# Kernel optimization log

Hardware: AMD Instinct MI355X
Metric: run time of the kernel (lower is better)

The kernel has to match this reference:

```python
import jax, jax.numpy as jnp
import numpy as np
from jax.scipy.special import xlogy

LAMBDA_XM = 0.05
LAMBDA_SEG2D = 1.0
BN_EPS = 1e-5


def setup_inputs() -> dict:
    key = jax.random.key(0)
    ks = jax.random.split(key, 40)
    S, N, Nv, B, Np, M, H, C, MID = 2, 240000, 80000, 2, 120000, 30000, 64, 20, 16
    Nimg = B * M
    f = lambda i, shape, s=0.05: jax.random.normal(ks[i], shape, jnp.float32) * s
    inp = {
        'img_feat': f(0, (S, Nimg, H), 1.0),
        'pts_feat': f(1, (S, Nv, H), 1.0),
        'coors_inv': jax.random.randint(ks[2], (S, N), 0, Nv),
        'labels': jax.random.randint(ks[3], (N,), 0, C),
        'img_label': jax.random.randint(ks[4], (Nimg,), 0, C),
        'p2img_idx': jax.random.randint(ks[5], (B, M), 0, Np),
        # multihead 3d classifiers (per scale): Linear(H,128)-ReLU-Linear(128,C)
        'w3a': f(6, (S, H, 128)), 'b3a': jnp.zeros((S, 128)),
        'w3b': f(7, (S, 128, C)), 'b3b': jnp.zeros((S, C)),
        # multihead fuse classifiers
        'wfa': f(8, (S, H, 128)), 'bfa': jnp.zeros((S, 128)),
        'wfb': f(9, (S, 128, C)), 'bfb': jnp.zeros((S, C)),
        # attention: fc1(H->H//4), fc2(H->H//4), fc3(H//2->2), conv1/conv2 (1x1 -> linear) + BN
        'fc1w': f(10, (S, H, MID)), 'fc1b': jnp.zeros((S, MID)),
        'fc2w': f(11, (S, H, MID)), 'fc2b': jnp.zeros((S, MID)),
        'fc3w': f(12, (S, 2 * MID, 2)), 'fc3b': jnp.zeros((S, 2)),
        'c1w': f(13, (S, H, H)), 'c1b': jnp.zeros((S, H)),
        'bn1g': jnp.ones((S, H)), 'bn1b': jnp.zeros((S, H)),
        'c2w': f(14, (S, H, H)), 'c2b': jnp.zeros((S, H)),
        'bn2g': jnp.ones((S, H)), 'bn2b': jnp.zeros((S, H)),
        # final classifier Linear(S*H,128)-ReLU-Linear(128,C)
        'clw1': f(15, (S * H, 128)), 'clb1': jnp.zeros((128,)),
        'clw2': f(16, (128, C)), 'clb2': jnp.zeros((C,)),
    }
    return inp


def _mlp2(x, w1, b1, w2, b2):
    return jax.nn.relu(x @ w1 + b1) @ w2 + b2


def _ce(logits, lab):
    logp = jax.nn.log_softmax(logits, -1)
    return -jnp.take_along_axis(logp, lab[:, None], axis=1).mean()


def _lovasz(probs, lab):
    # lovasz-softmax over all classes, averaged over present classes
    C = probs.shape[1]
    fg = jax.nn.one_hot(lab, C, dtype=probs.dtype)  # [N,C]
    errors = jnp.abs(fg - probs)

    def per_class(err_c, fg_c):
        order = jnp.argsort(-err_c)
        e = err_c[order]
        f = fg_c[order]
        gts = f.sum()
        inter = gts - jnp.cumsum(f)
        union = gts + jnp.cumsum(1.0 - f)
        jac = 1.0 - inter / union
        jac = jnp.concatenate([jac[:1], jac[1:] - jac[:-1]])
        return jnp.dot(e, jac)

    losses = jax.vmap(per_class)(errors.T, fg.T)  # [C]
    present = (fg.sum(0) > 0).astype(probs.dtype)
    return jnp.sum(losses * present) / jnp.maximum(present.sum(), 1.0)


def _seg_loss(logits, lab):
    return _ce(logits, lab) + _lovasz(jax.nn.softmax(logits, -1), lab)


def _convbn_relu(x, cw, cb, g, b):
    # 1x1 Conv1d == per-point linear; BN (training-mode batch stats over points)
    y = x @ cw + cb
    mu = y.mean(0)
    var = y.var(0)
    return jax.nn.relu((y - mu) * jax.lax.rsqrt(var + BN_EPS) * g + b)


def reference(img_feat, pts_feat, coors_inv, labels, img_label, p2img_idx,
              w3a, b3a, w3b, b3b, wfa, bfa, wfb, bfb,
              fc1w, fc1b, fc2w, fc2b, fc3w, fc3b,
              c1w, c1b, bn1g, bn1b, c2w, c2b, bn2g, bn2b,
              clw1, clb1, clw2, clb2):
    S, Nv, H = pts_feat.shape
    C = w3b.shape[-1]
    B, M = p2img_idx.shape
    N = labels.shape[0]
    Np = N // B
    # p2img_mapping: per-batch gather composed to one global gather (batch blocks are contiguous/equal)
    gidx = (jnp.arange(B)[:, None] * Np + p2img_idx).reshape(-1)  # [Nimg]

    loss = jnp.float32(0.0)
    feats = []
    for s in range(S):
        pred3d = _mlp2(pts_feat[s], w3a[s], b3a[s], w3b[s], b3b[s])  # [Nv,C]
        # voxelize_labels: majority vote per voxel (== unique+scatter_max count argmax)
        counts = jnp.zeros((Nv, C), jnp.float32).at[coors_inv[s], labels].add(1.0)
        vox_lab = jnp.argmax(counts, axis=1)  # [Nv]
        # gather voxel feats/preds to image-projected points (fused gather)
        idx = coors_inv[s][gidx]  # [Nimg]
        p = pts_feat[s][idx]      # [Nimg,H] pseudo feats
        pts_pred = pred3d[idx]    # [Nimg,C]
        v = img_feat[s]           # [Nimg,H] valid (image) feats
        # Attention fusion
        w = jax.nn.sigmoid(
            jnp.concatenate([p @ fc1w[s] + fc1b[s], v @ fc2w[s] + fc2b[s]], -1) @ fc3w[s] + fc3b[s])  # [Nimg,2]
        fuse = (_convbn_relu(p, c1w[s], c1b[s], bn1g[s], bn1b[s]) * w[:, 0:1]
                + _convbn_relu(v, c2w[s], c2b[s], bn2g[s], bn2b[s]) * w[:, 1:2])
        feats.append(fuse)
        fuse_pred = _mlp2(fuse, wfa[s], bfa[s], wfb[s], bfb[s])
        loss = loss + _seg_loss(pred3d, vox_lab)
        loss = loss + _seg_loss(fuse_pred, img_label) * LAMBDA_SEG2D / S
        # F.kl_div(log_softmax(pts_pred), softmax(fuse_pred)), reduction='mean' over all elements
        pf = jax.nn.softmax(fuse_pred, -1)
        kl = jnp.mean(xlogy(pf, pf) - pf * jax.nn.log_softmax(pts_pred, -1))
        loss = loss + kl * LAMBDA_XM / S
    img_logits = _mlp2(jnp.concatenate(feats, -1), clw1, clb1, clw2, clb2)
    loss = loss + _seg_loss(img_logits, img_label)
    return loss
```

## Files before the change

kernel.cpp:

```cpp
#include <hip/hip_runtime.h>
#include <stdint.h>

static constexpr int NV   = 80000;
static constexpr int NPT  = 240000;
static constexpr int NIMG = 60000;
static constexpr int Hh   = 64;
static constexpr int Cc   = 20;
static constexpr int NPp  = 120000;
static constexpr int Mm   = 30000;
static constexpr int NB     = 8192;
static constexpr int NCH    = 16;
static constexpr int NBLK_GA  = (NIMG + 63) / 64;
static constexpr int NBLK_MLP = NV / 64;
static constexpr int NBLK_CNT = (NPT + 255) / 256;
static constexpr int NBLK_FILL_NV = (NV + 255) / 256;
static constexpr int NBLK_FILL_NI = (NIMG + 255) / 256;
static constexpr int NBLK_HIST = Cc * NCH;
static constexpr int NBLK_GATH = 2 * NIMG * 8 / 256;
static constexpr int NBLK_P3G  = (2 * NIMG + 255) / 256;
#define BN_EPS 1e-5f

using bf16x8 = __attribute__((ext_vector_type(8))) short;
using f32x4  = __attribute__((ext_vector_type(4))) float;

__device__ __forceinline__ float waveReduce(float v) {
  #pragma unroll
  for (int o = 32; o > 0; o >>= 1) v += __shfl_down(v, o);
  return v;
}
__device__ __forceinline__ short f2bf(float f) {
  uint32_t u = __float_as_uint(f);
  return (short)((u + 0x7FFFu + ((u >> 16) & 1u)) >> 16);
}
__device__ __forceinline__ float bf2f(uint32_t h) { return __uint_as_float(h << 16); }
__device__ __forceinline__ uint32_t pk2(float a, float b) {
  return ((uint32_t)(uint16_t)f2bf(a)) | ((uint32_t)(uint16_t)f2bf(b) << 16);
}

struct PackDesc { const float* src; short* dst; int K, Nr, nt; };
struct PackArgs { PackDesc d[14]; };

__global__ void __launch_bounds__(256)
k_pack_zero(PackArgs pa,
            const float* __restrict__ fc1w, const float* __restrict__ fc1b,
            const float* __restrict__ fc2w, const float* __restrict__ fc2b,
            const float* __restrict__ fc3w, const float* __restrict__ fc3b,
            float* __restrict__ attEffs,
            uint4* __restrict__ zb, int zq,
            const int* __restrict__ ci0, const int* __restrict__ ci1,
            const int* __restrict__ p2img,
            int* __restrict__ idx0, int* __restrict__ idx1,
            const float* __restrict__ pts, uint16_t* __restrict__ pgath) {
  int bid = blockIdx.x;
  if (bid >= 384) {
    int g = (bid - 384) * 256 + threadIdx.x;
    int row = g >> 3, q = g & 7;
    int r = (row >= NIMG) ? row - NIMG : row;
    int s1 = (row >= NIMG) ? 1 : 0;
    const int* ci = s1 ? ci1 : ci0;
    int b = (r >= Mm) ? 1 : 0;
    int id = ci[b * NPp + p2img[r]];
    if (q == 0) { if (s1) idx1[r] = id; else idx0[r] = id; }
    const float* src = pts + (size_t)s1 * NV * 64 + (size_t)id * 64 + q * 8;
    float4 a = *(const float4*)src;
    float4 c = *(const float4*)(src + 4);
    uint4 o;
    o.x = pk2(a.x, a.y); o.y = pk2(a.z, a.w);
    o.z = pk2(c.x, c.y); o.w = pk2(c.z, c.w);
    *(uint4*)(pgath + (size_t)row * 64 + q * 8) = o;
    return;
  }
  if (bid >= 128) {
    const uint4 z = make_uint4(0u, 0u, 0u, 0u);
    int i = (bid - 128) * 256 + threadIdx.x;
    for (; i < zq; i += 256 * 256) zb[i] = z;
    return;
  }
  const int stride = 128 * 256;
  for (int di = 0; di < 14; di++) {
    const float* src = pa.d[di].src;
    short* dst = pa.d[di].dst;
    int K = pa.d[di].K, Nr = pa.d[di].Nr, ntiles = pa.d[di].nt;
    int total = (K / 32) * ntiles * 512;
    for (int idx = bid * 256 + threadIdx.x; idx < total; idx += stride) {
      int j = idx & 7, lane = (idx >> 3) & 63, tile = idx >> 9;
      int nt = tile % ntiles, kt = tile / ntiles;
      int k = kt * 32 + (lane >> 4) * 8 + j;
      int n = nt * 16 + (lane & 15);
      float v = (n < Nr) ? src[(size_t)k * Nr + n] : 0.f;
      dst[idx] = f2bf(v);
    }
  }
  if (bid < 2 && threadIdx.x < 64) {
    int s = bid, t = threadIdx.x;
    const float* f1w = fc1w + s * 64 * 16; const float* f1b = fc1b + s * 16;
    const float* f2w = fc2w + s * 64 * 16; const float* f2b = fc2b + s * 16;
    const float* f3w = fc3w + s * 64;      const float* f3b = fc3b + s * 2;
    float* aE = attEffs + s * 320;
    float p0 = 0.f, p1 = 0.f, v0 = 0.f, v1 = 0.f;
    #pragma unroll
    for (int j = 0; j < 16; j++) {
      p0 = fmaf(f1w[t * 16 + j], f3w[j * 2], p0);
      p1 = fmaf(f1w[t * 16 + j], f3w[j * 2 + 1], p1);
      v0 = fmaf(f2w[t * 16 + j], f3w[(16 + j) * 2], v0);
      v1 = fmaf(f2w[t * 16 + j], f3w[(16 + j) * 2 + 1], v1);
    }
    aE[t * 2] = p0; aE[t * 2 + 1] = p1;
    aE[128 + t * 2] = v0; aE[128 + t * 2 + 1] = v1;
    if (t == 0) {
      float b0 = f3b[0], b1 = f3b[1];
      for (int j = 0; j < 16; j++) {
        b0 += f1b[j] * f3w[j * 2] + f2b[j] * f3w[(16 + j) * 2];
        b1 += f1b[j] * f3w[j * 2 + 1] + f2b[j] * f3w[(16 + j) * 2 + 1];
      }
      aE[256] = b0; aE[257] = b1;
    }
  }
}

__device__ void scanbin_body(const unsigned long long* __restrict__ H64,
                             int n, int call, float* __restrict__ lossesC5,
                             int* __restrict__ gts5, int cls) {
  __shared__ int sWC[4], sWF[4];
  __shared__ float sRedF[4];
  int t = threadIdx.x;
  int lane = t & 63, w = t >> 6;
  const uint4* Hv = (const uint4*)(H64 + (size_t)cls * NB + (size_t)t * 32);
  int locC = 0, locF = 0;
  #pragma unroll
  for (int i = 0; i < 16; i++) {
    uint4 u = Hv[i];
    locF += (int)(u.x + u.z);
    locC += (int)(u.y + u.w);
  }
  int sc = locC, sf = locF;
  #pragma unroll
  for (int o = 1; o < 64; o <<= 1) {
    int a = __shfl_up(sc, o);
    int b = __shfl_up(sf, o);
    if (lane >= o) { sc += a; sf += b; }
  }
  if (lane == 63) { sWC[w] = sc; sWF[w] = sf; }
  __syncthreads();
  int offC = 0, offF = 0, Ftot = 0;
  #pragma unroll
  for (int ww = 0; ww < 4; ww++) {
    int fc = sWF[ww];
    Ftot += fc;
    if (ww < w) { offC += sWC[ww]; offF += fc; }
  }
  int runC = offC + sc - locC;
  int runF = offF + sf - locF;
  float gts = (float)Ftot;
  float contrib = 0.f;
  #pragma unroll
  for (int i = 0; i < 16; i++) {
    uint4 u = Hv[i];
    #pragma unroll
    for (int j = 0; j < 2; j++) {
      int cnt = (int)(j ? u.w : u.y), fgc = (int)(j ? u.z : u.x);
      runC += cnt; runF += fgc;
      if (cnt > 0 && Ftot > 0) {
        float r0 = (float)(n - runC);
        float F0 = (float)(Ftot - runF);
        float r1 = r0 + (float)cnt;
        float F1 = F0 + (float)fgc;
        float emean = __uint_as_float((uint32_t)(t * 32 + i * 2 + j) << 17);
        contrib += emean * (r1 / (gts + r1 - F1) - r0 / (gts + r0 - F0));
      }
    }
  }
  contrib = waveReduce(contrib);
  if (lane == 0) sRedF[w] = contrib;
  __syncthreads();
  if (t == 0) {
    lossesC5[call * 32 + cls] = (Ftot > 0) ? (sRedF[0] + sRedF[1] + sRedF[2] + sRedF[3]) : 0.f;
    gts5[call * 32 + cls] = Ftot;
  }
}

__device__ void tile_loss(const float* __restrict__ sL, int r0, int rows, int n,
                          const int* __restrict__ lab, uint16_t* __restrict__ E,
                          float ceScale, float* __restrict__ lossAcc) {
  int t = threadIdx.x;
  if (t < 64) {
    float total = 0.f;
    int gr = r0 + t;
    if (gr < rows) {
      const float* l = sL + t * 21;
      float m = l[0];
      #pragma unroll
      for (int c = 1; c < Cc; c++) m = fmaxf(m, l[c]);
      float ex[Cc]; float se = 0.f;
      #pragma unroll
      for (int c = 0; c < Cc; c++) { ex[c] = expf(l[c] - m); se += ex[c]; }
      float inv = 1.f / se;
      float lse = logf(se);
      int lb = lab[gr];
      total = -(l[lb] - m - lse) * ceScale;
      #pragma unroll
      for (int c = 0; c < Cc; c++) {
        float prob = ex[c] * inv;
        int fg = (c == lb) ? 1 : 0;
        float err = fg ? (1.f - prob) : prob;
        err = fmaxf(err, 0.f);
        uint32_t key = __float_as_uint(err) >> 17;
        E[(size_t)c * n + gr] = (uint16_t)((key << 1) | (uint32_t)fg);
      }
    }
    total = waveReduce(total);
    if (t == 0) atomicAdd(lossAcc, total);
  }
}

template<int D, bool TO_LDS>
__device__ __forceinline__ void mfma_mlp_core(const short* sXb, short* sH, float* sL,
    int r0, int rows,
    const short* __restrict__ pw1, const float* __restrict__ B1,
    const short* __restrict__ pw2, const float* __restrict__ B2,
    float* __restrict__ Out) {
  constexpr int LDB = D + 8;
  constexpr int KT1 = D / 32;
  const int t = threadIdx.x;
  const int lane = t & 63, w = t >> 6;
  const int m = lane & 15, quad = lane >> 4;
  const int rowA = 16 * w + m;
  bf16x8 a1[KT1];
  #pragma unroll
  for (int kt = 0; kt < KT1; kt++)
    a1[kt] = *(const bf16x8*)(sXb + rowA * LDB + kt * 32 + quad * 8);
  __syncthreads();
  const bf16x8* b1 = (const bf16x8*)pw1;
  #pragma unroll
  for (int nt = 0; nt < 8; nt++) {
    f32x4 c = {0.f, 0.f, 0.f, 0.f};
    #pragma unroll
    for (int kt = 0; kt < KT1; kt++)
      c = __builtin_amdgcn_mfma_f32_16x16x32_bf16(a1[kt], b1[(kt * 8 + nt) * 64 + lane], c, 0, 0, 0);
    int col = nt * 16 + m;
    float bc = B1[col];
    #pragma unroll
    for (int reg = 0; reg < 4; reg++)
      sH[(16 * w + quad * 4 + reg) * 136 + col] = f2bf(fmaxf(c[reg] + bc, 0.f));
  }
  __syncthreads();
  bf16x8 a2[4];
  #pragma unroll
  for (int kt = 0; kt < 4; kt++)
    a2[kt] = *(const bf16x8*)(sH + rowA * 136 + kt * 32 + quad * 8);
  if (TO_LDS) __syncthreads();
  const bf16x8* b2 = (const bf16x8*)pw2;
  #pragma unroll
  for (int nt = 0; nt < 2; nt++) {
    f32x4 c = {0.f, 0.f, 0.f, 0.f};
    #pragma unroll
    for (int kt = 0; kt < 4; kt++)
      c = __builtin_amdgcn_mfma_f32_16x16x32_bf16(a2[kt], b2[(kt * 2 + nt) * 64 + lane], c, 0, 0, 0);
    int col = nt * 16 + m;
    if (col < Cc) {
      float bc = B2[col];
      #pragma unroll
      for (int reg = 0; reg < 4; reg++) {
        int rr = 16 * w + quad * 4 + reg;
        if (TO_LDS) {
          sL[rr * 21 + col] = c[reg] + bc;
        } else {
          int gr = r0 + rr;
          if (gr < rows) Out[(size_t)gr * Cc + col] = c[reg] + bc;
        }
      }
    }
  }
}

__device__ void mlp64_body(int bid0, const float* __restrict__ X,
    const short* __restrict__ pw1, const float* __restrict__ B1,
    const short* __restrict__ pw2, const float* __restrict__ B2,
    float* __restrict__ Out, int rows, char* smem) {
  short* buf = (short*)smem;
  int t = threadIdx.x, r0 = bid0 * 64;
  for (int i = t; i < 1024; i += 256) {
    int r = i >> 4, k4 = (i & 15) * 4;
    int gr = r0 + r;
    float4 v = (gr < rows) ? *(const float4*)(X + (size_t)gr * 64 + k4)
                           : make_float4(0.f, 0.f, 0.f, 0.f);
    uint2 p; p.x = pk2(v.x, v.y); p.y = pk2(v.z, v.w);
    *(uint2*)(buf + r * 72 + k4) = p;
  }
  __syncthreads();
  mfma_mlp_core<64, false>(buf, buf, nullptr, r0, rows, pw1, B1, pw2, B2, Out);
}

__device__ void mlp128_loss_body(int bid0, const uint16_t* __restrict__ Xh,
    const short* __restrict__ pw1, const float* __restrict__ B1,
    const short* __restrict__ pw2, const float* __restrict__ B2,
    const int* __restrict__ lab, uint16_t* __restrict__ E, float ce,
    float* __restrict__ lossAcc, char* smem) {
  short* buf = (short*)smem;
  int t = threadIdx.x, r0 = bid0 * 64;
  for (int i = t; i < 2048; i += 256) {
    int r = i >> 5, k4 = (i & 31) * 4;
    int gr = r0 + r;
    uint2 p = (gr < NIMG) ? *(const uint2*)(Xh + (size_t)gr * 128 + k4) : make_uint2(0u, 0u);
    *(uint2*)(buf + r * 136 + k4) = p;
  }
  __syncthreads();
  mfma_mlp_core<128, true>(buf, buf, (float*)buf, r0, NIMG, pw1, B1, pw2, B2, nullptr);
  __syncthreads();
  tile_loss((float*)buf, r0, NIMG, NIMG, lab, E, ce, lossAcc);
}

__device__ void cnt_body(int bid0, const int* __restrict__ ci, const int* __restrict__ labels,
                         int* __restrict__ counts) {
  int i = bid0 * 256 + threadIdx.x;
  if (i < NPT) atomicAdd(&counts[(size_t)ci[i] * Cc + labels[i]], 1);
}

__device__ void colred_body(int bid0, const float* __restrict__ partials,
                            float* __restrict__ red64) {
  int t = threadIdx.x, j = bid0;
  float v = 0.f;
  for (int b = j; b < NBLK_GA; b += 64) v += partials[(size_t)b * 256 + t];
  red64[j * 256 + t] = v;
}

__device__ void p3gath_body(int bid0, const float* __restrict__ pred3d0,
                            const float* __restrict__ pred3d1,
                            const int* __restrict__ idx0, const int* __restrict__ idx1,
                            float* __restrict__ p3g0, float* __restrict__ p3g1) {
  int row = bid0 * 256 + threadIdx.x;
  if (row >= 2 * NIMG) return;
  int s1 = (row >= NIMG) ? 1 : 0;
  int r = s1 ? row - NIMG : row;
  const float* pred = s1 ? pred3d1 : pred3d0;
  float* dst = (s1 ? p3g1 : p3g0) + (size_t)r * Cc;
  const float* src = pred + (size_t)(s1 ? idx1[r] : idx0[r]) * Cc;
  #pragma unroll
  for (int c = 0; c < Cc; c += 2) {
    uint2 v = *(const uint2*)(src + c);
    *(uint2*)(dst + c) = v;
  }
}

__device__ void fill_body(int bid0, const float* __restrict__ logits,
                          const int* __restrict__ lab, const int* __restrict__ vcnt,
                          int n, uint16_t* __restrict__ E,
                          float ceScale, float* __restrict__ lossAcc,
                          const float* __restrict__ p3g, float klScale) {
  int i = bid0 * 256 + threadIdx.x;
  float total = 0.f;
  if (i < n) {
    int lb;
    if (vcnt) {
      const int* crow = vcnt + (size_t)i * Cc;
      int best = crow[0], arg = 0;
      #pragma unroll
      for (int k = 1; k < Cc; k++) {
        int ck = crow[k];
        if (ck > best) { best = ck; arg = k; }
      }
      lb = arg;
    } else {
      lb = lab[i];
    }
    const float* l = logits + (size_t)i * Cc;
    float m = l[0];
    #pragma unroll
    for (int c = 1; c < Cc; c++) m = fmaxf(m, l[c]);
    float ex[Cc]; float se = 0.f;
    #pragma unroll
    for (int c = 0; c < Cc; c++) { ex[c] = expf(l[c] - m); se += ex[c]; }
    float inv = 1.f / se;
    float lse = logf(se);
    total = -(l[lb] - m - lse) * ceScale;
    #pragma unroll
    for (int c = 0; c < Cc; c++) {
      float prob = ex[c] * inv;
      int fg = (c == lb) ? 1 : 0;
      float err = fg ? (1.f - prob) : prob;
      err = fmaxf(err, 0.f);
      uint32_t key = __float_as_uint(err) >> 17;
      E[(size_t)c * n + i] = (uint16_t)((key << 1) | (uint32_t)fg);
    }
    if (p3g) {
      const float* q = p3g + (size_t)i * Cc;
      float mq = q[0];
      #pragma unroll
      for (int c = 1; c < Cc; c++) mq = fmaxf(mq, q[c]);
      float sq = 0.f;
      #pragma unroll
      for (int c = 0; c < Cc; c++) sq += expf(q[c] - mq);
      float lsq = logf(sq);
      float kl = 0.f;
      #pragma unroll
      for (int c = 0; c < Cc; c++) {
        float lf = l[c] - m - lse;
        float pf = ex[c] * inv;
        float lq = q[c] - mq - lsq;
        kl += pf * (lf - lq);
      }
      total += kl * klScale;
    }
  }
  total = waveReduce(total);
  __shared__ float sh[4];
  int lane = threadIdx.x & 63, w = threadIdx.x >> 6;
  if (lane == 0) sh[w] = total;
  __syncthreads();
  if (threadIdx.x == 0) atomicAdd(lossAcc, sh[0] + sh[1] + sh[2] + sh[3]);
}

__device__ void hist_body(int bid0, const uint16_t* __restrict__ E, int n,
                          unsigned long long* __restrict__ H64, char* smem) {
  uint32_t* lcf = (uint32_t*)smem;
  int t = threadIdx.x;
  int cls = bid0 / NCH, ch = bid0 - cls * NCH;
  int CHsz = (n + NCH - 1) / NCH;
  int i0 = ch * CHsz;
  int i1 = min(n, i0 + CHsz);
  for (int b = t; b < NB; b += 256) lcf[b] = 0u;
  __syncthreads();
  const uint16_t* Ec = E + (size_t)cls * n;
  for (int i = i0 + t; i < i1; i += 256) {
    uint32_t p = Ec[i];
    atomicAdd(&lcf[p >> 1], 0x10000u | (p & 1u));
  }
  __syncthreads();
  unsigned long long* Hc = H64 + (size_t)cls * NB;
  for (int b = t; b < NB; b += 256) {
    uint32_t v = lcf[b];
    if (v)
      atomicAdd(&Hc[b], ((unsigned long long)(v >> 16) << 32) | (v & 0xFFFFu));
  }
}

__device__ void gatt_body(int bid0, const uint16_t* __restrict__ pg,
                          const float* __restrict__ img,
                          const short* __restrict__ pc1, const float* __restrict__ c1b,
                          const short* __restrict__ pc2, const float* __restrict__ c2b,
                          const float* __restrict__ attEff,
                          uint16_t* __restrict__ y1, uint16_t* __restrict__ y2,
                          float* __restrict__ attw, float* __restrict__ partials,
                          char* smem) {
  short* sP = (short*)smem;
  short* sV = (short*)(smem + 9216);
  float* sAtt  = (float*)(smem + 18432);
  float* sStat = (float*)smem;
  int t = threadIdx.x;
  int r0 = bid0 * 64;
  for (int i = t; i < 512; i += 256) {
    int r = i >> 3, q = i & 7;
    int gr = r0 + r;
    uint4 pv = make_uint4(0u, 0u, 0u, 0u);
    if (gr < NIMG) pv = *(const uint4*)(pg + (size_t)gr * 64 + q * 8);
    *(uint4*)(sP + r * 72 + q * 8) = pv;
  }
  for (int i = t; i < 1024; i += 256) {
    int r = i >> 4, q = i & 15;
    int gr = r0 + r;
    float4 vv = make_float4(0.f, 0.f, 0.f, 0.f);
    if (gr < NIMG) vv = *(const float4*)(img + (size_t)gr * 64 + q * 4);
    uint2 qv;
    qv.x = pk2(vv.x, vv.y); qv.y = pk2(vv.z, vv.w);
    *(uint2*)(sV + r * 72 + q * 4) = qv;
  }
  __syncthreads();
  {
    int r = t & 63, qq = t >> 6;
    const float* aP = attEff;
    const float* aV = attEff + 128;
    float l0 = 0.f, l1 = 0.f;
    for (int k = qq * 16; k < qq * 16 + 16; k += 4) {
      uint2 up = *(const uint2*)(sP + r * 72 + k);
      uint2 uv = *(const uint2*)(sV + r * 72 + k);
      float p0 = bf2f(up.x & 0xffff), p1 = bf2f(up.x >> 16);
      float p2 = bf2f(up.y & 0xffff), p3 = bf2f(up.y >> 16);
      float v0 = bf2f(uv.x & 0xffff), v1 = bf2f(uv.x >> 16);
      float v2 = bf2f(uv.y & 0xffff), v3 = bf2f(uv.y >> 16);
      float4 wa = *(const float4*)(aP + 2 * k);
      float4 wb = *(const float4*)(aP + 2 * k + 4);
      l0 += p0 * wa.x + p1 * wa.z + p2 * wb.x + p3 * wb.z;
      l1 += p0 * wa.y + p1 * wa.w + p2 * wb.y + p3 * wb.w;
      float4 ua = *(const float4*)(aV + 2 * k);
      float4 ub = *(const float4*)(aV + 2 * k + 4);
      l0 += v0 * ua.x + v1 * ua.z + v2 * ub.x + v3 * ub.z;
      l1 += v0 * ua.y + v1 * ua.w + v2 * ub.y + v3 * ub.w;
    }
    sAtt[r * 8 + qq * 2] = l0;
    sAtt[r * 8 + qq * 2 + 1] = l1;
  }
  const int lane = t & 63, w = t >> 6;
  const int m = lane & 15, quad = lane >> 4;
  const int rowA = 16 * w + m;
  bf16x8 ap[2], av[2];
  #pragma unroll
  for (int kt = 0; kt < 2; kt++) {
    ap[kt] = *(const bf16x8*)(sP + rowA * 72 + kt * 32 + quad * 8);
    av[kt] = *(const bf16x8*)(sV + rowA * 72 + kt * 32 + quad * 8);
  }
  __syncthreads();
  const bf16x8* b1 = (const bf16x8*)pc1;
  const bf16x8* b2 = (const bf16x8*)pc2;
  #pragma unroll
  for (int nt = 0; nt < 4; nt++) {
    int col = nt * 16 + m;
    f32x4 c1 = {0.f, 0.f, 0.f, 0.f}, c2 = {0.f, 0.f, 0.f, 0.f};
    #pragma unroll
    for (int kt = 0; kt < 2; kt++) {
      c1 = __builtin_amdgcn_mfma_f32_16x16x32_bf16(ap[kt], b1[(kt * 4 + nt) * 64 + lane], c1, 0, 0, 0);
      c2 = __builtin_amdgcn_mfma_f32_16x16x32_bf16(av[kt], b2[(kt * 4 + nt) * 64 + lane], c2, 0, 0, 0);
    }
    float bb1 = c1b[col], bb2 = c2b[col];
    float s1 = 0.f, q1 = 0.f, s2 = 0.f, q2 = 0.f;
    #pragma unroll
    for (int reg = 0; reg < 4; reg++) {
      int gr = r0 + 16 * w + quad * 4 + reg;
      if (gr < NIMG) {
        float v1 = c1[reg] + bb1, v2 = c2[reg] + bb2;
        y1[(size_t)gr * 64 + col] = (uint16_t)f2bf(v1);
        y2[(size_t)gr * 64 + col] = (uint16_t)f2bf(v2);
        s1 += v1; q1 = fmaf(v1, v1, q1);
        s2 += v2; q2 = fmaf(v2, v2, q2);
      }
    }
    s1 += __shfl_down(s1, 32); s1 += __shfl_down(s1, 16);
    q1 += __shfl_down(q1, 32); q1 += __shfl_down(q1, 16);
    s2 += __shfl_down(s2, 32); s2 += __shfl_down(s2, 16);
    q2 += __shfl_down(q2, 32); q2 += __shfl_down(q2, 16);
    if (lane < 16) {
      float* base = sStat + (w * 4 + nt) * 64 + lane;
      base[0]  = s1;
      base[16] = q1;
      base[32] = s2;
      base[48] = q2;
    }
  }
  __syncthreads();
  {
    int kind = t >> 6, col = t & 63;
    int nt = col >> 4, mm = col & 15;
    float v = 0.f;
    #pragma unroll
    for (int ww = 0; ww < 4; ww++)
      v += sStat[(ww * 4 + nt) * 64 + kind * 16 + mm];
    partials[(size_t)bid0 * 256 + kind * 64 + col] = v;
  }
  if (t < 64) {
    int gr = r0 + t;
    if (gr < NIMG) {
      float l0 = attEff[256] + sAtt[t * 8] + sAtt[t * 8 + 2] + sAtt[t * 8 + 4] + sAtt[t * 8 + 6];
      float l1 = attEff[257] + sAtt[t * 8 + 1] + sAtt[t * 8 + 3] + sAtt[t * 8 + 5] + sAtt[t * 8 + 7];
      attw[gr * 2]     = 1.f / (1.f + expf(-l0));
      attw[gr * 2 + 1] = 1.f / (1.f + expf(-l1));
    }
  }
}

__device__ void fusemlp_body(int bid0,
    const uint16_t* __restrict__ y1, const uint16_t* __restrict__ y2,
    const float* __restrict__ attw, const float* __restrict__ red64,
    const float* __restrict__ g1, const float* __restrict__ be1,
    const float* __restrict__ g2, const float* __restrict__ be2,
    uint16_t* __restrict__ feats, int s64,
    const short* __restrict__ pw1, const float* __restrict__ B1,
    const short* __restrict__ pw2, const float* __restrict__ B2,
    float* __restrict__ Out, char* smem) {
  short* buf = (short*)smem;
  float* sBn = (float*)(smem + 17408);
  int t = threadIdx.x, r0 = bid0 * 64;
  float acc = 0.f;
  #pragma unroll 8
  for (int b = 0; b < 64; b++) acc += red64[b * 256 + t];
  float* sSum = (float*)buf;
  sSum[t] = acc;
  __syncthreads();
  if (t < 64) {
    float nn = (float)NIMG;
    float mu1 = sSum[t] / nn;
    float var1 = sSum[64 + t] / nn - mu1 * mu1;
    float a1 = g1[t] / sqrtf(var1 + BN_EPS);
    sBn[t] = a1; sBn[64 + t] = be1[t] - mu1 * a1;
    float mu2 = sSum[128 + t] / nn;
    float var2 = sSum[192 + t] / nn - mu2 * mu2;
    float a2 = g2[t] / sqrtf(var2 + BN_EPS);
    sBn[128 + t] = a2; sBn[192 + t] = be2[t] - mu2 * a2;
  }
  __syncthreads();
  for (int i = t; i < 1024; i += 256) {
    int r = i >> 4, q = i & 15;
    int gr = r0 + r;
    uint2 zp = make_uint2(0u, 0u);
    if (gr < NIMG) {
      float4 a1 = *(const float4*)(sBn + q * 4);
      float4 c1 = *(const float4*)(sBn + 64 + q * 4);
      float4 a2 = *(const float4*)(sBn + 128 + q * 4);
      float4 c2 = *(const float4*)(sBn + 192 + q * 4);
      uint2 u1 = *(const uint2*)(y1 + (size_t)gr * 64 + q * 4);
      uint2 u2 = *(const uint2*)(y2 + (size_t)gr * 64 + q * 4);
      float w0 = attw[gr * 2], w1 = attw[gr * 2 + 1];
      float zx = fmaxf(fmaf(bf2f(u1.x & 0xffff), a1.x, c1.x), 0.f) * w0
               + fmaxf(fmaf(bf2f(u2.x & 0xffff), a2.x, c2.x), 0.f) * w1;
      float zy = fmaxf(fmaf(bf2f(u1.x >> 16),   a1.y, c1.y), 0.f) * w0
               + fmaxf(fmaf(bf2f(u2.x >> 16),   a2.y, c2.y), 0.f) * w1;
      float zz = fmaxf(fmaf(bf2f(u1.y & 0xffff), a1.z, c1.z), 0.f) * w0
               + fmaxf(fmaf(bf2f(u2.y & 0xffff), a2.z, c2.z), 0.f) * w1;
      float zw = fmaxf(fmaf(bf2f(u1.y >> 16),   a1.w, c1.w), 0.f) * w0
               + fmaxf(fmaf(bf2f(u2.y >> 16),   a2.w, c2.w), 0.f) * w1;
      zp.x = pk2(zx, zy); zp.y = pk2(zz, zw);
      *(uint2*)(feats + (size_t)gr * 128 + s64 + q * 4) = zp;
    }
    *(uint2*)(buf + r * 72 + q * 4) = zp;
  }
  __syncthreads();
  mfma_mlp_core<64, false>(buf, buf, nullptr, r0, NIMG, pw1, B1, pw2, B2, Out);
}

__global__ void __launch_bounds__(256)
k_mega2(const float* __restrict__ pf0, const float* __restrict__ pf1,
        const uint16_t* __restrict__ pg0, const uint16_t* __restrict__ pg1,
        const float* __restrict__ if0, const float* __restrict__ if1,
        const short* pc1w0, const short* pc1w1, const short* pc2w0, const short* pc2w1,
        const float* c1b, const float* c2b, const float* attEffs,
        uint16_t* y1a, uint16_t* y2a, uint16_t* y1b, uint16_t* y2b,
        float* attw0, float* attw1, float* partials0, float* partials1,
        const short* pw3a0, const float* b3a, const short* pw3b0, const float* b3b,
        const short* pw3a1, const short* pw3b1,
        float* pred3d0, float* pred3d1,
        const int* __restrict__ ci0, const int* __restrict__ ci1,
        const int* __restrict__ labels,
        int* __restrict__ counts0, int* __restrict__ counts1) {
  __shared__ char smem[20480];
  int bid = blockIdx.x;
  if (bid < NBLK_GA) {
    gatt_body(bid, pg0, if0, pc1w0, c1b, pc2w0, c2b, attEffs,
              y1a, y2a, attw0, partials0, smem);
    return;
  }
  bid -= NBLK_GA;
  if (bid < NBLK_GA) {
    gatt_body(bid, pg1, if1, pc1w1, c1b + 64, pc2w1, c2b + 64, attEffs + 320,
              y1b, y2b, attw1, partials1, smem);
    return;
  }
  bid -= NBLK_GA;
  if (bid < NBLK_MLP) { mlp64_body(bid, pf0, pw3a0, b3a, pw3b0, b3b, pred3d0, NV, smem); return; }
  bid -= NBLK_MLP;
  if (bid < NBLK_MLP) { mlp64_body(bid, pf1, pw3a1, b3a + 128, pw3b1, b3b + Cc, pred3d1, NV, smem); return; }
  bid -= NBLK_MLP;
  if (bid < NBLK_CNT) { cnt_body(bid, ci0, labels, counts0); return; }
  cnt_body(bid - NBLK_CNT, ci1, labels, counts1);
}

__global__ void __launch_bounds__(256)
k_colred_p3g(const float* partials0, float* red64_0,
             const float* partials1, float* red64_1,
             const float* __restrict__ pred3d0, const float* __restrict__ pred3d1,
             const int* __restrict__ idx0, const int* __restrict__ idx1,
             float* __restrict__ p3g0, float* __restrict__ p3g1) {
  int bid = blockIdx.x;
  if (bid < 64) { colred_body(bid, partials0, red64_0); return; }
  bid -= 64;
  if (bid < 64) { colred_body(bid, partials1, red64_1); return; }
  p3gath_body(bid - 64, pred3d0, pred3d1, idx0, idx1, p3g0, p3g1);
}

__global__ void __launch_bounds__(256)
k_fuse2_fill2(const uint16_t* y1a, const uint16_t* y2a, const float* attw0, const float* red64_0,
              const uint16_t* y1b, const uint16_t* y2b, const float* attw1, const float* red64_1,
              const float* bn1g, const float* bn1b, const float* bn2g, const float* bn2b,
              uint16_t* feats,
              const short* pwfa0, const float* bfa, const short* pwfb0, const float* bfb,
              const short* pwfa1, const short* pwfb1,
              float* fusepred0, float* fusepred1,
              const float* __restrict__ pred3d0, const int* __restrict__ counts0,
              uint16_t* __restrict__ E0,
              const float* __restrict__ pred3d1, const int* __restrict__ counts1,
              uint16_t* __restrict__ E1,
              float ceNV, float* lossAcc) {
  __shared__ char smem[18432];
  int bid = blockIdx.x;
  if (bid < NBLK_GA) {
    fusemlp_body(bid, y1a, y2a, attw0, red64_0, bn1g, bn1b, bn2g, bn2b, feats, 0,
                 pwfa0, bfa, pwfb0, bfb, fusepred0, smem);
    return;
  }
  bid -= NBLK_GA;
  if (bid < NBLK_GA) {
    fusemlp_body(bid, y1b, y2b, attw1, red64_1, bn1g + 64, bn1b + 64, bn2g + 64, bn2b + 64,
                 feats, 64, pwfa1, bfa + 128, pwfb1, bfb + Cc, fusepred1, smem);
    return;
  }
  bid -= NBLK_GA;
  if (bid < NBLK_FILL_NV) {
    fill_body(bid, pred3d0, nullptr, counts0, NV, E0, ceNV, lossAcc, nullptr, 0.f);
    return;
  }
  fill_body(bid - NBLK_FILL_NV, pred3d1, nullptr, counts1, NV, E1, ceNV, lossAcc, nullptr, 0.f);
}

__global__ void __launch_bounds__(256)
k_finx2(const uint16_t* __restrict__ feats,
        const short* pcl1, const float* clb1, const short* pcl2, const float* clb2,
        const int* __restrict__ img_label, uint16_t* E2, float ce4, float* lossAcc,
        const float* fusepred0, const float* p3g0, uint16_t* E3,
        const float* fusepred1, const float* p3g1, uint16_t* E4,
        float ce, float kl,
        const uint16_t* __restrict__ E0, unsigned long long* H0,
        const uint16_t* __restrict__ E1, unsigned long long* H2) {
  __shared__ char smem[32768];
  int bid = blockIdx.x;
  if (bid < NBLK_GA) {
    mlp128_loss_body(bid, feats, pcl1, clb1, pcl2, clb2, img_label, E2, ce4, lossAcc, smem);
    return;
  }
  bid -= NBLK_GA;
  if (bid < NBLK_FILL_NI) {
    fill_body(bid, fusepred0, img_label, nullptr, NIMG, E3, ce, lossAcc, p3g0, kl);
    return;
  }
  bid -= NBLK_FILL_NI;
  if (bid < NBLK_FILL_NI) {
    fill_body(bid, fusepred1, img_label, nullptr, NIMG, E4, ce, lossAcc, p3g1, kl);
    return;
  }
  bid -= NBLK_FILL_NI;
  if (bid < NBLK_HIST) { hist_body(bid, E0, NV, H0, smem); return; }
  hist_body(bid - NBLK_HIST, E1, NV, H2, smem);
}

__global__ void __launch_bounds__(256)
k_hist3_scan2(const uint16_t* __restrict__ E3, unsigned long long* H1,
              const uint16_t* __restrict__ E4, unsigned long long* H3,
              const uint16_t* __restrict__ E2, unsigned long long* H4,
              const unsigned long long* H0, const unsigned long long* H2s,
              float* lossesC5, int* gts5) {
  __shared__ char smem[32768];
  int bid = blockIdx.x;
  if (bid < NBLK_HIST) { hist_body(bid, E3, NIMG, H1, smem); return; }
  bid -= NBLK_HIST;
  if (bid < NBLK_HIST) { hist_body(bid, E4, NIMG, H3, smem); return; }
  bid -= NBLK_HIST;
  if (bid < NBLK_HIST) { hist_body(bid, E2, NIMG, H4, smem); return; }
  bid -= NBLK_HIST;
  if (bid < Cc) { scanbin_body(H0, NV, 0, lossesC5, gts5, bid); return; }
  scanbin_body(H2s, NV, 2, lossesC5, gts5, bid - Cc);
}

__global__ void __launch_bounds__(256)
k_scan3(const unsigned long long* H1, const unsigned long long* H3,
        const unsigned long long* H4,
        float* lossesC5, int* gts5) {
  int bid = blockIdx.x;
  if (bid < Cc) { scanbin_body(H1, NIMG, 1, lossesC5, gts5, bid); return; }
  bid -= Cc;
  if (bid < Cc) { scanbin_body(H3, NIMG, 3, lossesC5, gts5, bid); return; }
  scanbin_body(H4, NIMG, 4, lossesC5, gts5, bid - Cc);
}

__global__ void k_final(const float* __restrict__ lossAcc,
                        const float* __restrict__ lossesC5, const int* __restrict__ gts5,
                        float* __restrict__ out) {
  const float coefs[5] = {1.0f, 0.5f, 1.0f, 0.5f, 1.0f};
  float loss = lossAcc[0];
  for (int call = 0; call < 5; call++) {
    float s = 0.f; int np = 0;
    for (int c = 0; c < Cc; c++)
      if (gts5[call * 32 + c] > 0) { s += lossesC5[call * 32 + c]; np++; }
    loss += coefs[call] * s / (float)(np > 0 ? np : 1);
  }
  out[0] = loss;
}

extern "C" void kernel_launch(void* const* d_in, const int* in_sizes, int n_in,
                              void* d_out, int out_size, void* d_ws, size_t ws_size,
                              hipStream_t stream) {
  const float* img_feat = (const float*)d_in[0];
  const float* pts_feat = (const float*)d_in[1];
  const int* coors_inv  = (const int*)d_in[2];
  const int* labels     = (const int*)d_in[3];
  const int* img_label  = (const int*)d_in[4];
  const int* p2img      = (const int*)d_in[5];
  const float* w3a = (const float*)d_in[6];
  const float* b3a = (const float*)d_in[7];
  const float* w3b = (const float*)d_in[8];
  const float* b3b = (const float*)d_in[9];
  const float* wfa = (const float*)d_in[10];
  const float* bfa = (const float*)d_in[11];
  const float* wfb = (const float*)d_in[12];
  const float* bfb = (const float*)d_in[13];
  const float* fc1w = (const float*)d_in[14];
  const float* fc1b = (const float*)d_in[15];
  const float* fc2w = (const float*)d_in[16];
  const float* fc2b = (const float*)d_in[17];
  const float* fc3w = (const float*)d_in[18];
  const float* fc3b = (const float*)d_in[19];
  const float* c1w  = (const float*)d_in[20];
  const float* c1b  = (const float*)d_in[21];
  const float* bn1g = (const float*)d_in[22];
  const float* bn1b = (const float*)d_in[23];
  const float* c2w  = (const float*)d_in[24];
  const float* c2b  = (const float*)d_in[25];
  const float* bn2g = (const float*)d_in[26];
  const float* bn2b = (const float*)d_in[27];
  const float* clw1 = (const float*)d_in[28];
  const float* clb1 = (const float*)d_in[29];
  const float* clw2 = (const float*)d_in[30];
  const float* clb2 = (const float*)d_in[31];
  (void)in_sizes; (void)n_in; (void)out_size; (void)ws_size;

  char* ws = (char*)d_ws;
  size_t off = 0;
  auto alloc = [&](size_t bytes) { void* p = ws + off; off += (bytes + 255) & ~(size_t)255; return p; };
  uint16_t* feats = (uint16_t*)alloc((size_t)NIMG * 128 * 2);
  uint16_t* pgath = (uint16_t*)alloc((size_t)2 * NIMG * 64 * 2);
  float* pred3d0 = (float*)alloc((size_t)NV * Cc * 4);
  float* pred3d1 = (float*)alloc((size_t)NV * Cc * 4);
  float* p3g0 = (float*)alloc((size_t)NIMG * Cc * 4);
  float* p3g1 = (float*)alloc((size_t)NIMG * Cc * 4);
  int* idx0 = (int*)alloc((size_t)NIMG * 4);
  int* idx1 = (int*)alloc((size_t)NIMG * 4);
  uint16_t* y1a = (uint16_t*)alloc((size_t)NIMG * Hh * 2);
  uint16_t* y2a = (uint16_t*)alloc((size_t)NIMG * Hh * 2);
  uint16_t* y1b = (uint16_t*)alloc((size_t)NIMG * Hh * 2);
  uint16_t* y2b = (uint16_t*)alloc((size_t)NIMG * Hh * 2);
  uint16_t* E0 = (uint16_t*)alloc((size_t)Cc * NV * 2);
  uint16_t* E1 = (uint16_t*)alloc((size_t)Cc * NV * 2);
  uint16_t* E2 = (uint16_t*)alloc((size_t)Cc * NIMG * 2);
  uint16_t* E3 = (uint16_t*)alloc((size_t)Cc * NIMG * 2);
  uint16_t* E4 = (uint16_t*)alloc((size_t)Cc * NIMG * 2);
  float* partials0 = (float*)alloc((size_t)NBLK_GA * 256 * 4);
  float* partials1 = (float*)alloc((size_t)NBLK_GA * 256 * 4);
  float* red64_0 = (float*)alloc(64 * 256 * 4);
  float* red64_1 = (float*)alloc(64 * 256 * 4);
  float* attw0 = (float*)alloc((size_t)NIMG * 2 * 4);
  float* attw1 = (float*)alloc((size_t)NIMG * 2 * 4);
  float* fusepred0 = (float*)alloc((size_t)NIMG * Cc * 4);
  float* fusepred1 = (float*)alloc((size_t)NIMG * Cc * 4);
  short* pwAll = (short*)alloc(86016 * 2);
  short* pw3a0 = pwAll,          * pw3a1 = pwAll + 8192;
  short* pwfa0 = pwAll + 16384,  * pwfa1 = pwAll + 24576;
  short* pw3b0 = pwAll + 32768,  * pw3b1 = pwAll + 36864;
  short* pwfb0 = pwAll + 40960,  * pwfb1 = pwAll + 45056;
  short* pcl1  = pwAll + 49152;
  short* pcl2  = pwAll + 65536;
  short* pc1w0 = pwAll + 69632,  * pc1w1 = pwAll + 73728;
  short* pc2w0 = pwAll + 77824,  * pc2w1 = pwAll + 81920;
  float* attEffs = (float*)alloc(2 * 320 * 4);
  size_t zsize = 1024 + (size_t)5 * Cc * NB * 8 + (size_t)2 * NV * Cc * 4;
  char* zbase = (char*)alloc(zsize);
  float* lossAcc  = (float*)zbase;
  float* lossesC5 = (float*)zbase + 32;
  int*   gts5     = (int*)((float*)zbase + 192);
  unsigned long long* Hbase = (unsigned long long*)(zbase + 1024);
  auto Hc = [&](int call) { return Hbase + (size_t)call * Cc * NB; };
  int* counts0 = (int*)(zbase + 1024 + (size_t)5 * Cc * NB * 8);
  int* counts1 = counts0 + (size_t)NV * Cc;
  int zq = (int)(zsize / 16);

  const float kl = 0.025f / ((float)NIMG * Cc);
  const float* pf0 = pts_feat;
  const float* pf1 = pts_feat + (size_t)NV * Hh;
  const float* if0 = img_feat;
  const float* if1 = img_feat + (size_t)NIMG * Hh;
  const int* ci0 = coors_inv;
  const int* ci1 = coors_inv + NPT;
  uint16_t* pg0 = pgath;
  uint16_t* pg1 = pgath + (size_t)NIMG * 64;

  PackArgs pa;
  pa.d[0]  = {w3a,        pw3a0, 64, 128, 8};
  pa.d[1]  = {w3a + 8192, pw3a1, 64, 128, 8};
  pa.d[2]  = {wfa,        pwfa0, 64, 128, 8};
  pa.d[3]  = {wfa + 8192, pwfa1, 64, 128, 8};
  pa.d[4]  = {w3b,        pw3b0, 128, 20, 2};
  pa.d[5]  = {w3b + 2560, pw3b1, 128, 20, 2};
  pa.d[6]  = {wfb,        pwfb0, 128, 20, 2};
  pa.d[7]  = {wfb + 2560, pwfb1, 128, 20, 2};
  pa.d[8]  = {clw1,       pcl1, 128, 128, 8};
  pa.d[9]  = {clw2,       pcl2, 128, 20, 2};
  pa.d[10] = {c1w,        pc1w0, 64, 64, 4};
  pa.d[11] = {c1w + 4096, pc1w1, 64, 64, 4};
  pa.d[12] = {c2w,        pc2w0, 64, 64, 4};
  pa.d[13] = {c2w + 4096, pc2w1, 64, 64, 4};
  k_pack_zero<<<384 + NBLK_GATH, 256, 0, stream>>>(
      pa, fc1w, fc1b, fc2w, fc2b, fc3w, fc3b, attEffs,
      (uint4*)zbase, zq, ci0, ci1, p2img, idx0, idx1, pts_feat, pgath);

  k_mega2<<<2 * NBLK_GA + 2 * NBLK_MLP + 2 * NBLK_CNT, 256, 0, stream>>>(
      pf0, pf1, pg0, pg1, if0, if1,
      pc1w0, pc1w1, pc2w0, pc2w1, c1b, c2b, attEffs,
      y1a, y2a, y1b, y2b, attw0, attw1, partials0, partials1,
      pw3a0, b3a, pw3b0, b3b, pw3a1, pw3b1, pred3d0, pred3d1,
      ci0, ci1, labels, counts0, counts1);

  k_colred_p3g<<<128 + NBLK_P3G, 256, 0, stream>>>(
      partials0, red64_0, partials1, red64_1,
      pred3d0, pred3d1, idx0, idx1, p3g0, p3g1);

  k_fuse2_fill2<<<2 * NBLK_GA + 2 * NBLK_FILL_NV, 256, 0, stream>>>(
      y1a, y2a, attw0, red64_0, y1b, y2b, attw1, red64_1,
      bn1g, bn1b, bn2g, bn2b, feats,
      pwfa0, bfa, pwfb0, bfb, pwfa1, pwfb1, fusepred0, fusepred1,
      pred3d0, counts0, E0, pred3d1, counts1, E1,
      1.0f / NV, lossAcc);

  k_finx2<<<NBLK_GA + 2 * NBLK_FILL_NI + 2 * NBLK_HIST, 256, 0, stream>>>(
      feats, pcl1, clb1, pcl2, clb2,
      img_label, E2, 1.0f / NIMG, lossAcc,
      fusepred0, p3g0, E3,
      fusepred1, p3g1, E4,
      0.5f / NIMG, kl,
      E0, Hc(0), E1, Hc(2));

  k_hist3_scan2<<<3 * NBLK_HIST + 2 * Cc, 256, 0, stream>>>(
      E3, Hc(1), E4, Hc(3), E2, Hc(4),
      Hc(0), Hc(2), lossesC5, gts5);

  k_scan3<<<3 * Cc, 256, 0, stream>>>(Hc(1), Hc(3), Hc(4), lossesC5, gts5);

  k_final<<<1, 1, 0, stream>>>(lossAcc, lossesC5, gts5, (float*)d_out);
}
```

Before: 339.0 us.

## Replace BN partials reduction kernel with atomics and fold gather into fuse launch

The per-block BatchNorm sum and sum-of-squares partials are now accumulated directly into a zeroed global buffer with float atomics, instead of being written out and reduced by a separate column-reduction kernel. The pred3d gather blocks move into the fuse/fill launch, which removes one kernel launch and one pass over the partials. Each fuse block now reads 256 floats instead of summing 64 rows of partials. The cost is atomic contention from about 940 blocks per scale on 256 addresses, and float summation order is no longer deterministic.

```diff
diff --git a/kernel.cpp b/kernel.cpp
--- a/kernel.cpp
+++ b/kernel.cpp
@@ -316,14 +316,6 @@
   if (i < NPT) atomicAdd(&counts[(size_t)ci[i] * Cc + labels[i]], 1);
 }
 
-__device__ void colred_body(int bid0, const float* __restrict__ partials,
-                            float* __restrict__ red64) {
-  int t = threadIdx.x, j = bid0;
-  float v = 0.f;
-  for (int b = j; b < NBLK_GA; b += 64) v += partials[(size_t)b * 256 + t];
-  red64[j * 256 + t] = v;
-}
-
 __device__ void p3gath_body(int bid0, const float* __restrict__ pred3d0,
                             const float* __restrict__ pred3d1,
                             const int* __restrict__ idx0, const int* __restrict__ idx1,
@@ -440,7 +432,7 @@
                           const short* __restrict__ pc2, const float* __restrict__ c2b,
                           const float* __restrict__ attEff,
                           uint16_t* __restrict__ y1, uint16_t* __restrict__ y2,
-                          float* __restrict__ attw, float* __restrict__ partials,
+                          float* __restrict__ attw, float* __restrict__ bnAcc,
                           char* smem) {
   short* sP = (short*)smem;
   short* sV = (short*)(smem + 9216);
@@ -543,7 +535,7 @@
     #pragma unroll
     for (int ww = 0; ww < 4; ww++)
       v += sStat[(ww * 4 + nt) * 64 + kind * 16 + mm];
-    partials[(size_t)bid0 * 256 + kind * 64 + col] = v;
+    unsafeAtomicAdd(&bnAcc[t], v);
   }
   if (t < 64) {
     int gr = r0 + t;
@@ -558,7 +550,7 @@
 
 __device__ void fusemlp_body(int bid0,
     const uint16_t* __restrict__ y1, const uint16_t* __restrict__ y2,
-    const float* __restrict__ attw, const float* __restrict__ red64,
+    const float* __restrict__ attw, const float* __restrict__ bnAcc,
     const float* __restrict__ g1, const float* __restrict__ be1,
     const float* __restrict__ g2, const float* __restrict__ be2,
     uint16_t* __restrict__ feats, int s64,
@@ -568,11 +560,8 @@
   short* buf = (short*)smem;
   float* sBn = (float*)(smem + 17408);
   int t = threadIdx.x, r0 = bid0 * 64;
-  float acc = 0.f;
-  #pragma unroll 8
-  for (int b = 0; b < 64; b++) acc += red64[b * 256 + t];
   float* sSum = (float*)buf;
-  sSum[t] = acc;
+  sSum[t] = bnAcc[t];
   __syncthreads();
   if (t < 64) {
     float nn = (float)NIMG;
@@ -622,7 +611,7 @@
         const short* pc1w0, const short* pc1w1, const short* pc2w0, const short* pc2w1,
         const float* c1b, const float* c2b, const float* attEffs,
         uint16_t* y1a, uint16_t* y2a, uint16_t* y1b, uint16_t* y2b,
-        float* attw0, float* attw1, float* partials0, float* partials1,
+        float* attw0, float* attw1, float* bnAcc0, float* bnAcc1,
         const short* pw3a0, const float* b3a, const short* pw3b0, const float* b3b,
         const short* pw3a1, const short* pw3b1,
         float* pred3d0, float* pred3d1,
@@ -633,13 +622,13 @@
   int bid = blockIdx.x;
   if (bid < NBLK_GA) {
     gatt_body(bid, pg0, if0, pc1w0, c1b, pc2w0, c2b, attEffs,
-              y1a, y2a, attw0, partials0, smem);
+              y1a, y2a, attw0, bnAcc0, smem);
     return;
   }
   bid -= NBLK_GA;
   if (bid < NBLK_GA) {
     gatt_body(bid, pg1, if1, pc1w1, c1b + 64, pc2w1, c2b + 64, attEffs + 320,
-              y1b, y2b, attw1, partials1, smem);
+              y1b, y2b, attw1, bnAcc1, smem);
     return;
   }
   bid -= NBLK_GA;
@@ -652,21 +641,8 @@
 }
 
 __global__ void __launch_bounds__(256)
-k_colred_p3g(const float* partials0, float* red64_0,
-             const float* partials1, float* red64_1,
-             const float* __restrict__ pred3d0, const float* __restrict__ pred3d1,
-             const int* __restrict__ idx0, const int* __restrict__ idx1,
-             float* __restrict__ p3g0, float* __restrict__ p3g1) {
-  int bid = blockIdx.x;
-  if (bid < 64) { colred_body(bid, partials0, red64_0); return; }
-  bid -= 64;
-  if (bid < 64) { colred_body(bid, partials1, red64_1); return; }
-  p3gath_body(bid - 64, pred3d0, pred3d1, idx0, idx1, p3g0, p3g1);
-}
-
-__global__ void __launch_bounds__(256)
-k_fuse2_fill2(const uint16_t* y1a, const uint16_t* y2a, const float* attw0, const float* red64_0,
-              const uint16_t* y1b, const uint16_t* y2b, const float* attw1, const float* red64_1,
+k_fuse2_fill2(const uint16_t* y1a, const uint16_t* y2a, const float* attw0, const float* bnAcc0,
+              const uint16_t* y1b, const uint16_t* y2b, const float* attw1, const float* bnAcc1,
               const float* bn1g, const float* bn1b, const float* bn2g, const float* bn2b,
               uint16_t* feats,
               const short* pwfa0, const float* bfa, const short* pwfb0, const float* bfb,
@@ -676,17 +652,19 @@
               uint16_t* __restrict__ E0,
               const float* __restrict__ pred3d1, const int* __restrict__ counts1,
               uint16_t* __restrict__ E1,
-              float ceNV, float* lossAcc) {
+              float ceNV, float* lossAcc,
+              const int* __restrict__ idx0, const int* __restrict__ idx1,
+              float* __restrict__ p3g0, float* __restrict__ p3g1) {
   __shared__ char smem[18432];
   int bid = blockIdx.x;
   if (bid < NBLK_GA) {
-    fusemlp_body(bid, y1a, y2a, attw0, red64_0, bn1g, bn1b, bn2g, bn2b, feats, 0,
+    fusemlp_body(bid, y1a, y2a, attw0, bnAcc0, bn1g, bn1b, bn2g, bn2b, feats, 0,
                  pwfa0, bfa, pwfb0, bfb, fusepred0, smem);
     return;
   }
   bid -= NBLK_GA;
   if (bid < NBLK_GA) {
-    fusemlp_body(bid, y1b, y2b, attw1, red64_1, bn1g + 64, bn1b + 64, bn2g + 64, bn2b + 64,
+    fusemlp_body(bid, y1b, y2b, attw1, bnAcc1, bn1g + 64, bn1b + 64, bn2g + 64, bn2b + 64,
                  feats, 64, pwfa1, bfa + 128, pwfb1, bfb + Cc, fusepred1, smem);
     return;
   }
@@ -695,7 +673,12 @@
     fill_body(bid, pred3d0, nullptr, counts0, NV, E0, ceNV, lossAcc, nullptr, 0.f);
     return;
   }
-  fill_body(bid - NBLK_FILL_NV, pred3d1, nullptr, counts1, NV, E1, ceNV, lossAcc, nullptr, 0.f);
+  bid -= NBLK_FILL_NV;
+  if (bid < NBLK_FILL_NV) {
+    fill_body(bid, pred3d1, nullptr, counts1, NV, E1, ceNV, lossAcc, nullptr, 0.f);
+    return;
+  }
+  p3gath_body(bid - NBLK_FILL_NV, pred3d0, pred3d1, idx0, idx1, p3g0, p3g1);
 }
 
 __global__ void __launch_bounds__(256)
@@ -828,10 +811,6 @@
   uint16_t* E2 = (uint16_t*)alloc((size_t)Cc * NIMG * 2);
   uint16_t* E3 = (uint16_t*)alloc((size_t)Cc * NIMG * 2);
   uint16_t* E4 = (uint16_t*)alloc((size_t)Cc * NIMG * 2);
-  float* partials0 = (float*)alloc((size_t)NBLK_GA * 256 * 4);
-  float* partials1 = (float*)alloc((size_t)NBLK_GA * 256 * 4);
-  float* red64_0 = (float*)alloc(64 * 256 * 4);
-  float* red64_1 = (float*)alloc(64 * 256 * 4);
   float* attw0 = (float*)alloc((size_t)NIMG * 2 * 4);
   float* attw1 = (float*)alloc((size_t)NIMG * 2 * 4);
   float* fusepred0 = (float*)alloc((size_t)NIMG * Cc * 4);
@@ -846,14 +825,16 @@
   short* pc1w0 = pwAll + 69632,  * pc1w1 = pwAll + 73728;
   short* pc2w0 = pwAll + 77824,  * pc2w1 = pwAll + 81920;
   float* attEffs = (float*)alloc(2 * 320 * 4);
-  size_t zsize = 1024 + (size_t)5 * Cc * NB * 8 + (size_t)2 * NV * Cc * 4;
+  size_t zsize = 4096 + (size_t)5 * Cc * NB * 8 + (size_t)2 * NV * Cc * 4;
   char* zbase = (char*)alloc(zsize);
   float* lossAcc  = (float*)zbase;
   float* lossesC5 = (float*)zbase + 32;
   int*   gts5     = (int*)((float*)zbase + 192);
-  unsigned long long* Hbase = (unsigned long long*)(zbase + 1024);
+  float* bnAcc0   = (float*)(zbase + 1536);
+  float* bnAcc1   = (float*)(zbase + 2560);
+  unsigned long long* Hbase = (unsigned long long*)(zbase + 4096);
   auto Hc = [&](int call) { return Hbase + (size_t)call * Cc * NB; };
-  int* counts0 = (int*)(zbase + 1024 + (size_t)5 * Cc * NB * 8);
+  int* counts0 = (int*)(zbase + 4096 + (size_t)5 * Cc * NB * 8);
   int* counts1 = counts0 + (size_t)NV * Cc;
   int zq = (int)(zsize / 16);
 
@@ -889,20 +870,17 @@
   k_mega2<<<2 * NBLK_GA + 2 * NBLK_MLP + 2 * NBLK_CNT, 256, 0, stream>>>(
       pf0, pf1, pg0, pg1, if0, if1,
       pc1w0, pc1w1, pc2w0, pc2w1, c1b, c2b, attEffs,
-      y1a, y2a, y1b, y2b, attw0, attw1, partials0, partials1,
+      y1a, y2a, y1b, y2b, attw0, attw1, bnAcc0, bnAcc1,
       pw3a0, b3a, pw3b0, b3b, pw3a1, pw3b1, pred3d0, pred3d1,
       ci0, ci1, labels, counts0, counts1);
 
-  k_colred_p3g<<<128 + NBLK_P3G, 256, 0, stream>>>(
-      partials0, red64_0, partials1, red64_1,
-      pred3d0, pred3d1, idx0, idx1, p3g0, p3g1);
-
-  k_fuse2_fill2<<<2 * NBLK_GA + 2 * NBLK_FILL_NV, 256, 0, stream>>>(
-      y1a, y2a, attw0, red64_0, y1b, y2b, attw1, red64_1,
+  k_fuse2_fill2<<<2 * NBLK_GA + 2 * NBLK_FILL_NV + NBLK_P3G, 256, 0, stream>>>(
+      y1a, y2a, attw0, bnAcc0, y1b, y2b, attw1, bnAcc1,
       bn1g, bn1b, bn2g, bn2b, feats,
       pwfa0, bfa, pwfb0, bfb, pwfa1, pwfb1, fusepred0, fusepred1,
       pred3d0, counts0, E0, pred3d1, counts1, E1,
-      1.0f / NV, lossAcc);
+      1.0f / NV, lossAcc,
+      idx0, idx1, p3g0, p3g1);
 
   k_finx2<<<NBLK_GA + 2 * NBLK_FILL_NI + 2 * NBLK_HIST, 256, 0, stream>>>(
       feats, pcl1, clb1, pcl2, clb2,
```

Result: slower. 347.4 us (+2.5%).
